# Performance work log

Hardware: AMD Instinct MI355X
Metric: run time of the kernel (lower is better)

## Reference

```python
import jax, jax.numpy as jnp
import numpy as np

N_NODES = 100000
N_EDGES = 3200000  # avg degree 32
D_IN = 128
D_OUT = 64
BN_EPS = 0.001


def setup_inputs() -> dict:
    key = jax.random.key(0)
    k1, k2, k3, k4, k5 = jax.random.split(key, 5)
    x = jax.random.normal(k1, (N_NODES, D_IN), dtype=jnp.float32)
    W = jax.random.normal(k2, (D_IN, D_OUT), dtype=jnp.float32) * 0.05
    edge_val = jax.random.uniform(k3, (N_EDGES,), dtype=jnp.float32)
    edge_src = jax.random.randint(k4, (N_EDGES,), 0, N_NODES, dtype=jnp.int32)
    edge_dst = jax.random.randint(k5, (N_EDGES,), 0, N_NODES, dtype=jnp.int32)
    return {"x": x, "W": W, "edge_val": edge_val,
            "edge_src": edge_src, "edge_dst": edge_dst}


def reference(x, W, edge_val, edge_src, edge_dst):
    # pre_sup = X @ W  (dense feature transform; dropout rate is 0 -> identity)
    pre_sup = x @ W  # [N, D_OUT]
    # support = A @ pre_sup, A given in COO form: A[dst, src] = edge_val
    msgs = edge_val[:, None] * pre_sup[edge_src]          # [E, D_OUT]
    out = jax.ops.segment_sum(msgs, edge_dst, num_segments=N_NODES)  # [N, D_OUT]
    # tf.nn.moments over all-but-last axis + batch_norm (no scale/offset, eps=1e-3)
    mean = jnp.mean(out, axis=0)
    var = jnp.var(out, axis=0)
    out = (out - mean) * jax.lax.rsqrt(var + BN_EPS)
    return jax.nn.relu(out)
```

## Files before the change

kernel.cpp:

```cpp
#include <hip/hip_runtime.h>
#include <stdint.h>

#define D_IN  128
#define D_OUT 64
#define BN_EPS 1e-3f

#define BIN_SHIFT 6
#define BIN_NODES 64
#define BIN_CAP   2560
#define CHUNK     8192
#define MAX_BINS  1600

typedef __attribute__((ext_vector_type(8))) short bf16x8;
typedef __attribute__((ext_vector_type(4))) float f32x4;

__device__ __forceinline__ ushort f32_to_bf16_rne(float f) {
  uint u = __float_as_uint(f);
  u += 0x7FFFu + ((u >> 16) & 1u);
  return (ushort)(u >> 16);
}
__device__ __forceinline__ float bf16_to_f32(ushort h) {
  return __uint_as_float((uint)h << 16);
}

__global__ __launch_bounds__(256) void gemm_mfma_kernel(
    const float* __restrict__ x, const float* __restrict__ W,
    ushort* __restrict__ pre16, int n_nodes, int n_tiles) {
  __shared__ ushort Wb[D_IN * D_OUT];
  const int t = threadIdx.x;
  for (int i = t; i < D_IN * D_OUT; i += 256) Wb[i] = f32_to_bf16_rne(W[i]);
  __syncthreads();

  const int lane = t & 63;
  const int wave = t >> 6;
  const int m = lane & 15;
  const int quad = lane >> 4;

  bf16x8 bfrag[4][4];
#pragma unroll
  for (int nt = 0; nt < 4; ++nt)
#pragma unroll
    for (int s = 0; s < 4; ++s)
#pragma unroll
      for (int j = 0; j < 8; ++j)
        bfrag[nt][s][j] =
            (short)Wb[(32 * s + quad * 8 + j) * D_OUT + nt * 16 + m];

  for (int tile = blockIdx.x; tile < n_tiles; tile += gridDim.x) {
    const int rbase = tile * 64 + wave * 16;
    const int row = rbase + m;
    const size_t rl = (size_t)min(row, n_nodes - 1);
    f32x4 acc0 = {0.f, 0.f, 0.f, 0.f}, acc1 = {0.f, 0.f, 0.f, 0.f};
    f32x4 acc2 = {0.f, 0.f, 0.f, 0.f}, acc3 = {0.f, 0.f, 0.f, 0.f};
#pragma unroll
    for (int s = 0; s < 4; ++s) {
      const float4 xa = *(const float4*)&x[rl * D_IN + s * 32 + quad * 8];
      const float4 xb = *(const float4*)&x[rl * D_IN + s * 32 + quad * 8 + 4];
      bf16x8 af;
      af[0] = (short)f32_to_bf16_rne(xa.x);
      af[1] = (short)f32_to_bf16_rne(xa.y);
      af[2] = (short)f32_to_bf16_rne(xa.z);
      af[3] = (short)f32_to_bf16_rne(xa.w);
      af[4] = (short)f32_to_bf16_rne(xb.x);
      af[5] = (short)f32_to_bf16_rne(xb.y);
      af[6] = (short)f32_to_bf16_rne(xb.z);
      af[7] = (short)f32_to_bf16_rne(xb.w);
      acc0 = __builtin_amdgcn_mfma_f32_16x16x32_bf16(af, bfrag[0][s], acc0, 0, 0, 0);
      acc1 = __builtin_amdgcn_mfma_f32_16x16x32_bf16(af, bfrag[1][s], acc1, 0, 0, 0);
      acc2 = __builtin_amdgcn_mfma_f32_16x16x32_bf16(af, bfrag[2][s], acc2, 0, 0, 0);
      acc3 = __builtin_amdgcn_mfma_f32_16x16x32_bf16(af, bfrag[3][s], acc3, 0, 0, 0);
    }
#pragma unroll
    for (int reg = 0; reg < 4; ++reg) {
      const int r = rbase + quad * 4 + reg;
      if (r < n_nodes) {
        ushort* po = &pre16[(size_t)r * D_OUT + m];
        po[0]  = f32_to_bf16_rne(acc0[reg]);
        po[16] = f32_to_bf16_rne(acc1[reg]);
        po[32] = f32_to_bf16_rne(acc2[reg]);
        po[48] = f32_to_bf16_rne(acc3[reg]);
      }
    }
  }
}

__global__ __launch_bounds__(256) void partition_kernel(
    const float* __restrict__ ev, const int* __restrict__ esrc,
    const int* __restrict__ edst, int* __restrict__ bin_cursor,
    uint2* __restrict__ bucket, int n_edges, int n_bins) {
  __shared__ int cnt[MAX_BINS];
  __shared__ int base[MAX_BINS];
  const int t = threadIdx.x;
  const int beg = blockIdx.x * CHUNK;
  const int end = min(beg + CHUNK, n_edges);

  for (int i = t; i < n_bins; i += 256) cnt[i] = 0;
  __syncthreads();

  for (int i = beg + t; i < end; i += 256)
    atomicAdd(&cnt[edst[i] >> BIN_SHIFT], 1);
  __syncthreads();

  for (int i = t; i < n_bins; i += 256) {
    const int c = cnt[i];
    int b = 0;
    if (c > 0) b = atomicAdd(&bin_cursor[i], c);
    if (b > BIN_CAP) b = BIN_CAP;
    base[i] = i * BIN_CAP + b;
    cnt[i] = 0;
  }
  __syncthreads();

  for (int i = beg + t; i < end; i += 256) {
    const int dst = edst[i];
    const int bin = dst >> BIN_SHIFT;
    const int r = atomicAdd(&cnt[bin], 1);
    const int pos = base[bin] + r;
    if (pos < (bin + 1) * BIN_CAP) {
      const uint w0 = ((uint)(dst & (BIN_NODES - 1)) << 17) | (uint)esrc[i];
      bucket[pos] = make_uint2(w0, __float_as_uint(ev[i]));
    }
  }
}

__global__ __launch_bounds__(256) void bin_sort_gather_kernel(
    const ushort* __restrict__ pre16, const uint2* __restrict__ bucket,
    const int* __restrict__ bin_cursor, float* __restrict__ out,
    float* __restrict__ stats, int n_nodes) {
  __shared__ uint s_src[BIN_CAP];
  __shared__ ushort s_val[BIN_CAP];
  __shared__ int s_hist[BIN_NODES];
  __shared__ int s_off[BIN_NODES + 1];
  __shared__ int s_cur[BIN_NODES];

  const int t = threadIdx.x;
  const int bin = blockIdx.x;
  const int cnt = min(bin_cursor[bin], BIN_CAP);
  const int64_t rbase = (int64_t)bin * BIN_CAP;

  if (t < BIN_NODES) s_hist[t] = 0;
  __syncthreads();

  for (int i = t; i < cnt; i += 256)
    atomicAdd(&s_hist[bucket[rbase + i].x >> 17], 1);
  __syncthreads();

  int own = (t < BIN_NODES) ? s_hist[t] : 0;
  for (int off = 1; off < BIN_NODES; off <<= 1) {
    int u = 0;
    if (t < BIN_NODES && t >= off) u = s_hist[t - off];
    __syncthreads();
    if (t < BIN_NODES) s_hist[t] += u;
    __syncthreads();
  }
  if (t < BIN_NODES) {
    const int e = s_hist[t] - own;
    s_off[t] = e;
    s_cur[t] = e;
  }
  if (t == 0) s_off[BIN_NODES] = cnt;
  __syncthreads();

  for (int i = t; i < cnt; i += 256) {
    const uint2 r = bucket[rbase + i];
    const int d = r.x >> 17;
    const int p = atomicAdd(&s_cur[d], 1);
    s_src[p] = r.x & 0x1FFFFu;
    s_val[p] = f32_to_bf16_rne(__uint_as_float(r.y));
  }
  __syncthreads();

  const int lane = t & 63;
  const int wave = t >> 6;
  const int half = lane >> 5;
  const int hl = lane & 31;
  const int node0 = bin * BIN_NODES;
  float csx = 0.f, csy = 0.f, cs2x = 0.f, cs2y = 0.f;

  for (int nl = wave; nl < BIN_NODES; nl += 4) {
    const int node = node0 + nl;
    if (node < n_nodes) {
      const int jb = s_off[nl], je = s_off[nl + 1];
      float a0x = 0.f, a0y = 0.f, a1x = 0.f, a1y = 0.f;
      int j = jb + half;
      for (; j + 2 < je; j += 4) {
        const uint src0 = s_src[j];
        const uint src1 = s_src[j + 2];
        const float v0 = bf16_to_f32(s_val[j]);
        const float v1 = bf16_to_f32(s_val[j + 2]);
        const uint p0 = *(const uint*)&pre16[(size_t)src0 * D_OUT + 2 * hl];
        const uint p1 = *(const uint*)&pre16[(size_t)src1 * D_OUT + 2 * hl];
        a0x += v0 * bf16_to_f32((ushort)(p0 & 0xFFFFu));
        a0y += v0 * bf16_to_f32((ushort)(p0 >> 16));
        a1x += v1 * bf16_to_f32((ushort)(p1 & 0xFFFFu));
        a1y += v1 * bf16_to_f32((ushort)(p1 >> 16));
      }
      if (j < je) {
        const uint src = s_src[j];
        const float v = bf16_to_f32(s_val[j]);
        const uint p = *(const uint*)&pre16[(size_t)src * D_OUT + 2 * hl];
        a0x += v * bf16_to_f32((ushort)(p & 0xFFFFu));
        a0y += v * bf16_to_f32((ushort)(p >> 16));
      }
      float ax = a0x + a1x, ay = a0y + a1y;
      ax += __shfl_xor(ax, 32);
      ay += __shfl_xor(ay, 32);
      if (half == 0) {
        *(float2*)&out[(size_t)node * D_OUT + 2 * hl] = make_float2(ax, ay);
        csx += ax;
        cs2x += ax * ax;
        csy += ay;
        cs2y += ay * ay;
      }
    }
  }
  __syncthreads();

  float* red = (float*)s_src;
  float* red2 = red + 256;
  if (half == 0) {
    red[wave * 64 + 2 * hl] = csx;
    red[wave * 64 + 2 * hl + 1] = csy;
    red2[wave * 64 + 2 * hl] = cs2x;
    red2[wave * 64 + 2 * hl + 1] = cs2y;
  }
  __syncthreads();
  if (t < 64) {
    float s = red[t] + red[64 + t] + red[128 + t] + red[192 + t];
    float s2 = red2[t] + red2[64 + t] + red2[128 + t] + red2[192 + t];
    atomicAdd(&stats[t], s);
    atomicAdd(&stats[64 + t], s2);
  }
}

__global__ __launch_bounds__(256) void norm_kernel(
    float* __restrict__ out, const float* __restrict__ stats, int64_t n_elems,
    float inv_n) {
  const int c = threadIdx.x & 63;
  const float mean = stats[c] * inv_n;
  const float var = stats[64 + c] * inv_n - mean * mean;
  const float scale = rsqrtf(var + BN_EPS);
  const int64_t stride = (int64_t)gridDim.x * 256;
  for (int64_t i = (int64_t)blockIdx.x * 256 + threadIdx.x; i < n_elems;
       i += stride) {
    const float v = (out[i] - mean) * scale;
    out[i] = v > 0.f ? v : 0.f;
  }
}

extern "C" void kernel_launch(void* const* d_in, const int* in_sizes, int n_in,
                              void* d_out, int out_size, void* d_ws,
                              size_t ws_size, hipStream_t stream) {
  const float* x = (const float*)d_in[0];
  const float* W = (const float*)d_in[1];
  const float* ev = (const float*)d_in[2];
  const int* esrc = (const int*)d_in[3];
  const int* edst = (const int*)d_in[4];

  const int n_nodes = in_sizes[0] / D_IN;
  const int n_edges = in_sizes[2];
  const int64_t n_out = (int64_t)n_nodes * D_OUT;
  const int n_bins = (n_nodes + BIN_NODES - 1) >> BIN_SHIFT;
  const int n_row_tiles = (n_nodes + 63) / 64;

  float* out = (float*)d_out;

  char* w = (char*)d_ws;
  ushort* pre16 = (ushort*)w;             w += (size_t)n_nodes * D_OUT * 2;
  int* bin_cursor = (int*)w;              w += (size_t)n_bins * 4;
  float* stats = (float*)w;               w += 128 * 4;
  w = (char*)(((uintptr_t)w + 7) & ~(uintptr_t)7);
  uint2* bucket = (uint2*)w;

  hipMemsetAsync(bin_cursor, 0, (size_t)n_bins * 4, stream);
  hipMemsetAsync(stats, 0, 128 * 4, stream);

  gemm_mfma_kernel<<<(n_row_tiles + 1) / 2, 256, 0, stream>>>(
      x, W, pre16, n_nodes, n_row_tiles);
  partition_kernel<<<(n_edges + CHUNK - 1) / CHUNK, 256, 0, stream>>>(
      ev, esrc, edst, bin_cursor, bucket, n_edges, n_bins);
  bin_sort_gather_kernel<<<n_bins, 256, 0, stream>>>(pre16, bucket, bin_cursor,
                                                     out, stats, n_nodes);
  norm_kernel<<<2048, 256, 0, stream>>>(out, stats, n_out,
                                        1.0f / (float)n_nodes);
}
```

Baseline: 346.3 us.

## Unroll gather loop deeper, vectorize norm kernel, enlarge partition chunk

The per-node gather loop now processes four edges per half-wave per iteration with four independent accumulator pairs, so more global loads are in flight at once. The normalization kernel reads and writes float4 instead of scalars, with four per-channel means and scales per thread. The partition chunk size is doubled so fewer blocks are launched. The deeper unroll raises register use, and larger chunks mean fewer blocks to spread the partition work across the GPU.

After: 353.4 us. +2.1%, slower.

```diff
diff --git a/kernel.cpp b/kernel.cpp
--- a/kernel.cpp
+++ b/kernel.cpp
@@ -8,7 +8,7 @@
 #define BIN_SHIFT 6
 #define BIN_NODES 64
 #define BIN_CAP   2560
-#define CHUNK     8192
+#define CHUNK     16384
 #define MAX_BINS  1600
 
 typedef __attribute__((ext_vector_type(8))) short bf16x8;
@@ -182,27 +182,37 @@
     if (node < n_nodes) {
       const int jb = s_off[nl], je = s_off[nl + 1];
       float a0x = 0.f, a0y = 0.f, a1x = 0.f, a1y = 0.f;
+      float a2x = 0.f, a2y = 0.f, a3x = 0.f, a3y = 0.f;
       int j = jb + half;
-      for (; j + 2 < je; j += 4) {
-        const uint src0 = s_src[j];
-        const uint src1 = s_src[j + 2];
+      for (; j + 6 < je; j += 8) {
+        const uint src0 = s_src[j],     src1 = s_src[j + 2];
+        const uint src2 = s_src[j + 4], src3 = s_src[j + 6];
         const float v0 = bf16_to_f32(s_val[j]);
         const float v1 = bf16_to_f32(s_val[j + 2]);
+        const float v2 = bf16_to_f32(s_val[j + 4]);
+        const float v3 = bf16_to_f32(s_val[j + 6]);
         const uint p0 = *(const uint*)&pre16[(size_t)src0 * D_OUT + 2 * hl];
         const uint p1 = *(const uint*)&pre16[(size_t)src1 * D_OUT + 2 * hl];
+        const uint p2 = *(const uint*)&pre16[(size_t)src2 * D_OUT + 2 * hl];
+        const uint p3 = *(const uint*)&pre16[(size_t)src3 * D_OUT + 2 * hl];
         a0x += v0 * bf16_to_f32((ushort)(p0 & 0xFFFFu));
         a0y += v0 * bf16_to_f32((ushort)(p0 >> 16));
         a1x += v1 * bf16_to_f32((ushort)(p1 & 0xFFFFu));
         a1y += v1 * bf16_to_f32((ushort)(p1 >> 16));
+        a2x += v2 * bf16_to_f32((ushort)(p2 & 0xFFFFu));
+        a2y += v2 * bf16_to_f32((ushort)(p2 >> 16));
+        a3x += v3 * bf16_to_f32((ushort)(p3 & 0xFFFFu));
+        a3y += v3 * bf16_to_f32((ushort)(p3 >> 16));
       }
-      if (j < je) {
+      for (; j < je; j += 2) {
         const uint src = s_src[j];
         const float v = bf16_to_f32(s_val[j]);
         const uint p = *(const uint*)&pre16[(size_t)src * D_OUT + 2 * hl];
         a0x += v * bf16_to_f32((ushort)(p & 0xFFFFu));
         a0y += v * bf16_to_f32((ushort)(p >> 16));
       }
-      float ax = a0x + a1x, ay = a0y + a1y;
+      float ax = (a0x + a1x) + (a2x + a3x);
+      float ay = (a0y + a1y) + (a2y + a3y);
       ax += __shfl_xor(ax, 32);
       ay += __shfl_xor(ay, 32);
       if (half == 0) {
@@ -234,17 +244,29 @@
 }
 
 __global__ __launch_bounds__(256) void norm_kernel(
-    float* __restrict__ out, const float* __restrict__ stats, int64_t n_elems,
+    float* __restrict__ out, const float* __restrict__ stats, int64_t n_vec4,
     float inv_n) {
-  const int c = threadIdx.x & 63;
-  const float mean = stats[c] * inv_n;
-  const float var = stats[64 + c] * inv_n - mean * mean;
-  const float scale = rsqrtf(var + BN_EPS);
+  const int c = (threadIdx.x * 4) & 63;
+  float mean[4], scale[4];
+#pragma unroll
+  for (int k = 0; k < 4; ++k) {
+    mean[k] = stats[c + k] * inv_n;
+    const float var = stats[64 + c + k] * inv_n - mean[k] * mean[k];
+    scale[k] = rsqrtf(var + BN_EPS);
+  }
   const int64_t stride = (int64_t)gridDim.x * 256;
-  for (int64_t i = (int64_t)blockIdx.x * 256 + threadIdx.x; i < n_elems;
+  for (int64_t i = (int64_t)blockIdx.x * 256 + threadIdx.x; i < n_vec4;
        i += stride) {
-    const float v = (out[i] - mean) * scale;
-    out[i] = v > 0.f ? v : 0.f;
+    float4 v = ((float4*)out)[i];
+    v.x = (v.x - mean[0]) * scale[0];
+    v.y = (v.y - mean[1]) * scale[1];
+    v.z = (v.z - mean[2]) * scale[2];
+    v.w = (v.w - mean[3]) * scale[3];
+    v.x = v.x > 0.f ? v.x : 0.f;
+    v.y = v.y > 0.f ? v.y : 0.f;
+    v.z = v.z > 0.f ? v.z : 0.f;
+    v.w = v.w > 0.f ? v.w : 0.f;
+    ((float4*)out)[i] = v;
   }
 }
 
@@ -281,6 +303,6 @@
       ev, esrc, edst, bin_cursor, bucket, n_edges, n_bins);
   bin_sort_gather_kernel<<<n_bins, 256, 0, stream>>>(pre16, bucket, bin_cursor,
                                                      out, stats, n_nodes);
-  norm_kernel<<<2048, 256, 0, stream>>>(out, stats, n_out,
+  norm_kernel<<<2048, 256, 0, stream>>>(out, stats, n_out / 4,
                                         1.0f / (float)n_nodes);
 }
```
